# Optimization experiments

Hardware: AMD Instinct MI355X
Metric: run time of the kernel (lower is better)

The kernel has to match this reference:

```python
import jax, jax.numpy as jnp
import numpy as np

WIN = 8
NUM_LAYERS = 2
HID = 512
GROUPS = 4
GH = 2 * HID // GROUPS  # 256


def _shuffle(y):
    # torch Shuffle: transpose(-1,-2).contiguous().view(original_shape)
    return jnp.swapaxes(y, -1, -2).reshape(y.shape)


def _gru_cell(xt, h, w_ih, w_hh, b_ih, b_hh):
    # torch.nn.GRUCell math; gate order r, z, n
    gi = xt @ w_ih.T + b_ih  # [B, 3H]
    gh = h @ w_hh.T + b_hh   # [B, 3H]
    i_r, i_z, i_n = jnp.split(gi, 3, axis=1)
    h_r, h_z, h_n = jnp.split(gh, 3, axis=1)
    r = jax.nn.sigmoid(i_r + h_r)
    z = jax.nn.sigmoid(i_z + h_z)
    n = jnp.tanh(i_n + r * h_n)
    return (1.0 - z) * n + z * h


def _sort_attn(h, a1, a2, a3, a4):
    B, H = h.shape
    s = jnp.sort(h, axis=1)                 # stable sort along features
    se = jnp.stack((h, s), axis=1)          # [B, 2, H]
    y = se @ a1.T                           # Linear(H, H) -> [B, 2, H]
    y = y.reshape(B, GROUPS, GH)            # Flatten + Unflatten
    y = _shuffle(y)
    y = y @ a2.T                            # Linear(GH, GH)
    y = _shuffle(y)
    y = jax.nn.relu(y @ a3.T)               # Linear(GH, GH) + ReLU
    y = y.reshape(B, GROUPS * GH)           # [B, 2H]
    scores = jax.nn.sigmoid(y @ a4.T)       # Linear(2H, H) -> [B, H]
    return h * scores


def setup_inputs() -> dict:
    key = jax.random.key(0)
    ks = jax.random.split(key, 10)
    B, L, C = 64, 4096, 64
    sc = 0.05
    inp = {
        "x": jax.random.normal(ks[0], (B, L, C), dtype=jnp.float32),
        "hidden0": jnp.zeros((NUM_LAYERS, 1, HID), dtype=jnp.float32),
        "w_ih": jax.random.normal(ks[1], (NUM_LAYERS, 3 * HID, HID), dtype=jnp.float32) * sc,
        "w_hh": jax.random.normal(ks[2], (NUM_LAYERS, 3 * HID, HID), dtype=jnp.float32) * sc,
        "b_ih": jax.random.normal(ks[3], (NUM_LAYERS, 3 * HID), dtype=jnp.float32) * sc,
        "b_hh": jax.random.normal(ks[4], (NUM_LAYERS, 3 * HID), dtype=jnp.float32) * sc,
        "a1": jax.random.normal(ks[5], (NUM_LAYERS, HID, HID), dtype=jnp.float32) * sc,
        "a2": jax.random.normal(ks[6], (NUM_LAYERS, GH, GH), dtype=jnp.float32) * sc,
        "a3": jax.random.normal(ks[7], (NUM_LAYERS, GH, GH), dtype=jnp.float32) * sc,
        "a4": jax.random.normal(ks[8], (NUM_LAYERS, HID, 2 * HID), dtype=jnp.float32) * sc,
    }
    return inp


def reference(x, hidden0, w_ih, w_hh, b_ih, b_hh, a1, a2, a3, a4):
    B, L, C = x.shape
    xp = x.reshape(B, L // WIN, WIN * C)
    xs = jnp.swapaxes(xp, 0, 1)                       # [T, B, D]
    h0 = jnp.broadcast_to(hidden0, (NUM_LAYERS, B, HID))

    def step(hid, xt):
        inp = xt
        new = []
        for l in range(NUM_LAYERS):
            h = _gru_cell(inp, hid[l], w_ih[l], w_hh[l], b_ih[l], b_hh[l])
            h = _sort_attn(h, a1[l], a2[l], a3[l], a4[l])
            new.append(h)
            inp = h
        return jnp.stack(new, axis=0), inp

    _, outs = jax.lax.scan(step, h0, xs)              # outs: [T, B, H]
    return jnp.swapaxes(outs, 0, 1)                   # [B, T, H]
```

## Files before the change

### kernel.cpp

```cpp
#include <hip/hip_runtime.h>

#define SCOPE_AGENT __HIP_MEMORY_SCOPE_AGENT

#define OFF_HS    0
#define OFF_HP    65536
#define OFF_SG    131072
#define OFF_U     196608
#define OFF_CTR   327680
#define OFF_T1    393216
#define OFF_M     2490368
#define OFF_GIX   4587520
#define OFF_XT    4587520
#define WS_GIX    54919168
#define WS_XT     21364736

__device__ __forceinline__ float sigm(float x) { return 1.f / (1.f + expf(-x)); }

__device__ __forceinline__ float ld_sc1(const float* p) {
    return __hip_atomic_load(p, __ATOMIC_RELAXED, SCOPE_AGENT);
}
__device__ __forceinline__ void st_sc1(float* p, float v) {
    __hip_atomic_store(p, v, __ATOMIC_RELAXED, SCOPE_AGENT);
}
__device__ __forceinline__ void ld2(const float* p, float& a, float& b) {
    unsigned long long v = __hip_atomic_load((const unsigned long long*)p,
                                             __ATOMIC_RELAXED, SCOPE_AGENT);
    a = __uint_as_float((unsigned)v);
    b = __uint_as_float((unsigned)(v >> 32));
}
__device__ __forceinline__ void st2(float* p, float a, float b) {
    unsigned long long v = ((unsigned long long)__float_as_uint(b) << 32) |
                           (unsigned long long)__float_as_uint(a);
    __hip_atomic_store((unsigned long long*)p, v, __ATOMIC_RELAXED, SCOPE_AGENT);
}

__device__ __forceinline__ void gbar(unsigned* flags, unsigned* genr, unsigned g) {
    __syncthreads();
    const int tid = threadIdx.x;
    if (blockIdx.x == 0) {
        if (tid >= 1 && tid < 256) {
            while (__hip_atomic_load(&flags[tid << 5], __ATOMIC_RELAXED, SCOPE_AGENT) < g)
                __builtin_amdgcn_s_sleep(1);
        }
        __syncthreads();
        if (tid < 16)
            __hip_atomic_store(&genr[tid << 5], g, __ATOMIC_RELAXED, SCOPE_AGENT);
        __syncthreads();
    } else {
        if (tid == 0) {
            __hip_atomic_store(&flags[blockIdx.x << 5], g, __ATOMIC_RELAXED, SCOPE_AGENT);
            while (__hip_atomic_load(&genr[(blockIdx.x & 15) << 5], __ATOMIC_RELAXED, SCOPE_AGENT) < g)
                __builtin_amdgcn_s_sleep(1);
        }
        __syncthreads();
    }
}

__global__ void k_init(const float* __restrict__ h0, float* __restrict__ ws) {
    int idx = blockIdx.x * blockDim.x + threadIdx.x;
    int l = idx >> 15, k = (idx & 32767) >> 6, lane = idx & 63;
    ws[OFF_HS + (l << 15) + ((k >> 1) << 7) + (lane << 1) + (k & 1)] = h0[(l << 9) + k];
    if (idx < 8704) ((unsigned*)(ws + OFF_CTR))[idx] = 0u;
}

__global__ void k_gix(const float* __restrict__ x, const float* __restrict__ wih,
                      float* __restrict__ gix) {
    __shared__ float xs[128][65];
    __shared__ float ww[32][129];
    int t = blockIdx.x, rb = blockIdx.y * 32;
    int tid = threadIdx.x;
    int rw = tid >> 6, b = tid & 63;
    float acc[8] = {0.f, 0.f, 0.f, 0.f, 0.f, 0.f, 0.f, 0.f};
    for (int kc = 0; kc < 4; kc++) {
        __syncthreads();
        for (int i = tid; i < 8192; i += 256) {
            int k = i & 127, b2 = i >> 7;
            xs[k][b2] = x[(size_t)b2 * 262144 + (size_t)t * 512 + kc * 128 + k];
        }
        for (int i = tid; i < 4096; i += 256) {
            int r = i >> 7, k = i & 127;
            ww[r][k] = wih[(size_t)(rb + r) * 512 + kc * 128 + k];
        }
        __syncthreads();
        for (int k = 0; k < 128; k++) {
            float xv = xs[k][b];
#pragma unroll
            for (int rr = 0; rr < 8; rr++)
                acc[rr] = fmaf(ww[rw * 8 + rr][k], xv, acc[rr]);
        }
    }
#pragma unroll
    for (int rr = 0; rr < 8; rr++) {
        int rg = rb + rw * 8 + rr;
        int g = rg >> 9, j = rg & 511;
        gix[((size_t)((size_t)t * 512 + j) * 3 + g) * 64 + b] = acc[rr];
    }
}

__global__ void k_xtk(const float* __restrict__ x, float* __restrict__ xT) {
    __shared__ float tile[64][65];
    int t = blockIdx.x >> 3, kc = blockIdx.x & 7;
    int k = threadIdx.x & 63, b0 = threadIdx.x >> 6;
    for (int i = 0; i < 16; i++) {
        int b = i * 4 + b0;
        tile[k][b] = x[(size_t)b * 262144 + (size_t)t * 512 + kc * 64 + k];
    }
    __syncthreads();
    int b2 = threadIdx.x & 63, k0 = threadIdx.x >> 6;
    for (int i = 0; i < 16; i++) {
        int k2 = i * 4 + k0;
        xT[((size_t)t * 512 + kc * 64 + k2) * 64 + b2] = tile[k2][b2];
    }
}

__global__ void k_t1(const float* __restrict__ a1, const float* __restrict__ a2,
                     float* __restrict__ T1) {
    int l = blockIdx.x >> 10, c = blockIdx.x & 1023;
    int g = c >> 8, jj = c & 255;
    __shared__ float sA2[256];
    sA2[threadIdx.x] = a2[l * 65536 + jj * 256 + threadIdx.x];
    __syncthreads();
    const float* A1l = a1 + l * 262144;
    for (int colq = 0; colq < 4; colq++) {
        int col = colq * 256 + threadIdx.x;
        int half = col >> 9, cm = col & 511;
        float acc = 0.f;
#pragma unroll 4
        for (int q = 0; q < 64; q++) {
            int a0 = 2 * half;
            int j0 = g * 64 + q;
            acc = fmaf(sA2[4 * q + a0],     A1l[j0 * 512 + cm], acc);
            acc = fmaf(sA2[4 * q + a0 + 1], A1l[(j0 + 256) * 512 + cm], acc);
        }
        T1[((size_t)(l << 10) + c) * 1024 + col] = acc;
    }
}

__global__ void k_m(const float* __restrict__ a3, const float* __restrict__ T1,
                    float* __restrict__ M) {
    int l = blockIdx.x >> 10, c = blockIdx.x & 1023;
    int g = c >> 8, jj = c & 255;
    __shared__ float sA3[256];
    sA3[threadIdx.x] = a3[l * 65536 + jj * 256 + threadIdx.x];
    __syncthreads();
    const float* T1l = T1 + ((size_t)l << 20);
    for (int colq = 0; colq < 4; colq++) {
        int col = colq * 256 + threadIdx.x;
        float acc = 0.f;
#pragma unroll 4
        for (int m = 0; m < 256; m++) {
            int p = ((m & 3) << 8) + (g << 6) + (m >> 2);
            acc = fmaf(sA3[m], T1l[p * 1024 + col], acc);
        }
        M[((size_t)(l << 10) + c) * 1024 + col] = acc;
    }
}

__global__ void __launch_bounds__(1024, 1)
persist(const float* __restrict__ x, const float* __restrict__ xT,
        const float* __restrict__ gix, int has_xt, int has_gix,
        const float* __restrict__ wih, const float* __restrict__ whh,
        const float* __restrict__ bih, const float* __restrict__ bhh,
        const float* __restrict__ Mc, const float* __restrict__ a4,
        float* __restrict__ ws, float* __restrict__ out) {
    __shared__ float wA[2][2][6][512];
    __shared__ float wM[2][4][1024];
    __shared__ float wD[2][2][1024];
    __shared__ float red2[12][16][64];
    __shared__ float bb[2][2][4];
    __shared__ float sH[2][2][64];

    const int tid = threadIdx.x, w = tid >> 6, lane = tid & 63, bid = blockIdx.x;

    for (int i = tid; i < 12288; i += 1024) {
        int l = i / 6144, r = i % 6144, f = r / 3072, r2 = r % 3072, d = r2 / 512, k = r2 & 511;
        int gate = d >> 1, side = d & 1;
        int j = 2 * bid + f;
        const float* src = side ? whh : wih;
        wA[l][f][d][k] = src[l * 786432 + (gate * 512 + j) * 512 + k];
    }
    for (int i = tid; i < 8192; i += 1024) {
        int l = i >> 12, r = (i >> 10) & 3, col = i & 1023;
        wM[l][r][col] = Mc[((size_t)(l << 10) + 4 * bid + r) * 1024 + col];
    }
    for (int i = tid; i < 4096; i += 1024) {
        int l = i >> 11, f = (i >> 10) & 1, k = i & 1023;
        wD[l][f][k] = a4[l * 524288 + (2 * bid + f) * 1024 + k];
    }
    if (tid < 16) {
        int l = tid / 8, f = (tid / 4) & 1, g = tid & 3;
        int j = 2 * bid + f;
        float v;
        if (g == 0)      v = bih[l * 1536 + j] + bhh[l * 1536 + j];
        else if (g == 1) v = bih[l * 1536 + 512 + j] + bhh[l * 1536 + 512 + j];
        else if (g == 2) v = bih[l * 1536 + 1024 + j];
        else             v = bhh[l * 1536 + 1024 + j];
        bb[l][f][g] = v;
    }
    __syncthreads();

    float* hsG = ws + OFF_HS;
    float* hPg = ws + OFF_HP;
    float* sGg = ws + OFF_SG;
    float* uG  = ws + OFF_U;
    unsigned* flags = (unsigned*)(ws + OFF_CTR);
    unsigned* genr  = flags + 8192;
    unsigned bgen = 0;

    auto stageA = [&](int l, int t) {
        float hprev = 0.f;
        if (w < 2) {
            int j = 2 * bid + w;
            hprev = ld_sc1(&hsG[(l << 15) + ((j >> 1) << 7) + (lane << 1) + (j & 1)]);
        }
        const float* hb = hsG + (l << 15);
        float* hPl = hPg + (l << 15);
        int k0 = w * 32;
        if (l == 0 && has_gix) {
            float acc[6] = {0.f, 0.f, 0.f, 0.f, 0.f, 0.f};
#pragma unroll 8
            for (int m = 0; m < 16; m++) {
                int k = k0 + 2 * m;
                float ha, hb2;
                ld2(&hb[(k >> 1) * 128 + lane * 2], ha, hb2);
#pragma unroll
                for (int f = 0; f < 2; f++) {
                    acc[f * 3 + 0] = fmaf(wA[0][f][1][k], ha, fmaf(wA[0][f][1][k + 1], hb2, acc[f * 3 + 0]));
                    acc[f * 3 + 1] = fmaf(wA[0][f][3][k], ha, fmaf(wA[0][f][3][k + 1], hb2, acc[f * 3 + 1]));
                    acc[f * 3 + 2] = fmaf(wA[0][f][5][k], ha, fmaf(wA[0][f][5][k + 1], hb2, acc[f * 3 + 2]));
                }
            }
#pragma unroll
            for (int u = 0; u < 6; u++) red2[u][w][lane] = acc[u];
            __syncthreads();
            if (w < 2) {
                int f = w, j = 2 * bid + f;
                float s0 = 0, s1 = 0, s2 = 0;
#pragma unroll
                for (int i = 0; i < 16; i++) {
                    s0 += red2[f * 3 + 0][i][lane];
                    s1 += red2[f * 3 + 1][i][lane];
                    s2 += red2[f * 3 + 2][i][lane];
                }
                const float* gx = gix + ((size_t)((size_t)t * 512 + j) * 3) * 64;
                float r = sigm(gx[lane] + s0 + bb[0][f][0]);
                float z = sigm(gx[64 + lane] + s1 + bb[0][f][1]);
                float n = tanhf(gx[128 + lane] + bb[0][f][2] + r * (s2 + bb[0][f][3]));
                float hp = (1.f - z) * n + z * hprev;
                sH[0][f][lane] = hp;
                st_sc1(&hPl[bid * 128 + lane * 2 + f], hp);
            }
        } else {
            float acc[12];
#pragma unroll
            for (int u = 0; u < 12; u++) acc[u] = 0.f;
#pragma unroll 8
            for (int m = 0; m < 16; m++) {
                int k = k0 + 2 * m;
                float ia, ib, ha, hb2;
                if (l == 1) {
                    ld2(&hsG[(k >> 1) * 128 + lane * 2], ia, ib);
                } else if (has_xt) {
                    ia = xT[(size_t)t * 32768 + k * 64 + lane];
                    ib = xT[(size_t)t * 32768 + (k + 1) * 64 + lane];
                } else {
                    ia = x[(size_t)lane * 262144 + (size_t)t * 512 + k];
                    ib = x[(size_t)lane * 262144 + (size_t)t * 512 + k + 1];
                }
                ld2(&hb[(k >> 1) * 128 + lane * 2], ha, hb2);
#pragma unroll
                for (int f = 0; f < 2; f++) {
                    acc[f * 6 + 0] = fmaf(wA[l][f][0][k], ia, fmaf(wA[l][f][0][k + 1], ib, acc[f * 6 + 0]));
                    acc[f * 6 + 1] = fmaf(wA[l][f][1][k], ha, fmaf(wA[l][f][1][k + 1], hb2, acc[f * 6 + 1]));
                    acc[f * 6 + 2] = fmaf(wA[l][f][2][k], ia, fmaf(wA[l][f][2][k + 1], ib, acc[f * 6 + 2]));
                    acc[f * 6 + 3] = fmaf(wA[l][f][3][k], ha, fmaf(wA[l][f][3][k + 1], hb2, acc[f * 6 + 3]));
                    acc[f * 6 + 4] = fmaf(wA[l][f][4][k], ia, fmaf(wA[l][f][4][k + 1], ib, acc[f * 6 + 4]));
                    acc[f * 6 + 5] = fmaf(wA[l][f][5][k], ha, fmaf(wA[l][f][5][k + 1], hb2, acc[f * 6 + 5]));
                }
            }
#pragma unroll
            for (int u = 0; u < 12; u++) red2[u][w][lane] = acc[u];
            __syncthreads();
            if (w < 2) {
                int f = w, j = 2 * bid + f;
                float g0 = 0, g1 = 0, g2 = 0, g3 = 0, g4 = 0, g5 = 0;
#pragma unroll
                for (int i = 0; i < 16; i++) {
                    g0 += red2[f * 6 + 0][i][lane]; g1 += red2[f * 6 + 1][i][lane];
                    g2 += red2[f * 6 + 2][i][lane]; g3 += red2[f * 6 + 3][i][lane];
                    g4 += red2[f * 6 + 4][i][lane]; g5 += red2[f * 6 + 5][i][lane];
                }
                float r = sigm(g0 + g1 + bb[l][f][0]);
                float z = sigm(g2 + g3 + bb[l][f][1]);
                float n = tanhf(g4 + bb[l][f][2] + r * (g5 + bb[l][f][3]));
                float hp = (1.f - z) * n + z * hprev;
                sH[l][f][lane] = hp;
                st_sc1(&hPl[bid * 128 + lane * 2 + f], hp);
            }
        }
    };

    auto stageB = [&](int l, float* accB) {
        int j0 = 2 * bid, j1 = j0 + 1;
        float v0 = sH[l][0][lane], v1 = sH[l][1][lane];
        const float* hPl = hPg + (l << 15);
        float* sGl = sGg + (l << 15);
        int k0 = w * 32, cnt0 = 0, cnt1 = 0;
        accB[0] = accB[1] = accB[2] = accB[3] = 0.f;
#pragma unroll 8
        for (int m = 0; m < 16; m++) {
            int k = k0 + 2 * m;
            float ha, hb2;
            ld2(&hPl[(k >> 1) * 128 + lane * 2], ha, hb2);
            cnt0 += (ha < v0 || (ha == v0 && k < j0)) ? 1 : 0;
            cnt0 += (hb2 < v0 || (hb2 == v0 && k + 1 < j0)) ? 1 : 0;
            cnt1 += (ha < v1 || (ha == v1 && k < j1)) ? 1 : 0;
            cnt1 += (hb2 < v1 || (hb2 == v1 && k + 1 < j1)) ? 1 : 0;
#pragma unroll
            for (int r = 0; r < 4; r++)
                accB[r] = fmaf(wM[l][r][k], ha, fmaf(wM[l][r][k + 1], hb2, accB[r]));
        }
        red2[0][w][lane] = (float)cnt0;
        red2[1][w][lane] = (float)cnt1;
        __syncthreads();
        if (w < 2) {
            int rk = 0;
#pragma unroll
            for (int i = 0; i < 16; i++) rk += (int)red2[w][i][lane];
            st_sc1(&sGl[rk * 64 + lane], sH[l][w][lane]);
        }
    };

    auto stageC = [&](int l, const float* accB) {
        float acc[4] = {accB[0], accB[1], accB[2], accB[3]};
        int s0 = w * 32;
        const float* sGl = sGg + (l << 15);
#pragma unroll 8
        for (int ss = 0; ss < 32; ss++) {
            int sp = s0 + ss;
            float vv = ld_sc1(&sGl[sp * 64 + lane]);
#pragma unroll
            for (int r = 0; r < 4; r++)
                acc[r] = fmaf(wM[l][r][512 + sp], vv, acc[r]);
        }
#pragma unroll
        for (int r = 0; r < 4; r++) red2[r][w][lane] = acc[r];
        __syncthreads();
        if (w < 2) {
            float sa = 0.f, sb = 0.f;
#pragma unroll
            for (int i = 0; i < 16; i++) {
                sa += red2[2 * w + 0][i][lane];
                sb += red2[2 * w + 1][i][lane];
            }
            st2(&uG[(l << 16) + (2 * bid + w) * 128 + lane * 2],
                fmaxf(sa, 0.f), fmaxf(sb, 0.f));
        }
    };

    auto stageD = [&](int l, int t) {
        float a0 = 0.f, a1v = 0.f;
        int k0 = w * 64;
        const float* uL = uG + (l << 16);
#pragma unroll 8
        for (int m = 0; m < 32; m++) {
            int k = k0 + 2 * m;
            float ua, ub;
            ld2(&uL[(k >> 1) * 128 + lane * 2], ua, ub);
            a0 = fmaf(wD[l][0][k], ua, fmaf(wD[l][0][k + 1], ub, a0));
            a1v = fmaf(wD[l][1][k], ua, fmaf(wD[l][1][k + 1], ub, a1v));
        }
        red2[0][w][lane] = a0;
        red2[1][w][lane] = a1v;
        __syncthreads();
        if (w < 2) {
            float s = 0.f;
#pragma unroll
            for (int i = 0; i < 16; i++) s += red2[w][i][lane];
            float hnew = sH[l][w][lane] * sigm(s);
            int j = 2 * bid + w;
            st_sc1(&hsG[(l << 15) + bid * 128 + lane * 2 + w], hnew);
            if (l == 1)
                out[(size_t)lane * 262144 + (size_t)t * 512 + j] = hnew;
        }
    };

    float accB0[4], accB1[4];

    for (int t = 0; t <= 512; t++) {
        const int t0 = t, t1 = t - 1;
        const bool do0 = (t0 < 512), do1 = (t1 >= 0);

        if (do0) stageA(0, t0);
        if (do1) { __syncthreads(); stageA(1, t1); }
        gbar(flags, genr, ++bgen);

        if (do0) stageB(0, accB0);
        if (do1) { __syncthreads(); stageB(1, accB1); }
        gbar(flags, genr, ++bgen);

        if (do0) stageC(0, accB0);
        if (do1) { __syncthreads(); stageC(1, accB1); }
        gbar(flags, genr, ++bgen);

        if (do0) stageD(0, t0);
        if (do1) { __syncthreads(); stageD(1, t1); }
        gbar(flags, genr, ++bgen);
    }
}

extern "C" void kernel_launch(void* const* d_in, const int* in_sizes, int n_in,
                              void* d_out, int out_size, void* d_ws, size_t ws_size,
                              hipStream_t stream) {
    const float* x   = (const float*)d_in[0];
    const float* h0  = (const float*)d_in[1];
    const float* wih = (const float*)d_in[2];
    const float* whh = (const float*)d_in[3];
    const float* bih = (const float*)d_in[4];
    const float* bhh = (const float*)d_in[5];
    const float* a1  = (const float*)d_in[6];
    const float* a2  = (const float*)d_in[7];
    const float* a3  = (const float*)d_in[8];
    const float* a4  = (const float*)d_in[9];
    float* ws  = (float*)d_ws;
    float* out = (float*)d_out;

    int has_gix = (ws_size >= (size_t)WS_GIX * 4) ? 1 : 0;
    int has_xt  = (!has_gix && ws_size >= (size_t)WS_XT * 4) ? 1 : 0;
    float* T1p = ws + OFF_T1;
    float* Mp  = ws + OFF_M;
    const float* gixp = ws + OFF_GIX;
    const float* xTp  = ws + OFF_XT;

    hipLaunchKernelGGL(k_init, dim3(256), dim3(256), 0, stream, h0, ws);
    if (has_gix)
        hipLaunchKernelGGL(k_gix, dim3(512, 48), dim3(256), 0, stream, x, wih, ws + OFF_GIX);
    else if (has_xt)
        hipLaunchKernelGGL(k_xtk, dim3(4096), dim3(256), 0, stream, x, ws + OFF_XT);
    hipLaunchKernelGGL(k_t1, dim3(2048), dim3(256), 0, stream, a1, a2, T1p);
    hipLaunchKernelGGL(k_m, dim3(2048), dim3(256), 0, stream, a3, T1p, Mp);

    void* args[] = {(void*)&x, (void*)&xTp, (void*)&gixp, (void*)&has_xt, (void*)&has_gix,
                    (void*)&wih, (void*)&whh, (void*)&bih, (void*)&bhh,
                    (void*)&Mp, (void*)&a4, (void*)&ws, (void*)&out};
    hipLaunchCooperativeKernel((void*)persist, dim3(256), dim3(1024), args, 0, stream);
}
```

Measured before the change: 45.07 ms.

## Switch global state buffers to 4-wide interleaved layout with batched dwordx4 loads

Changes the layout of the hidden-state, sorted and intermediate global buffers from pairs of features per lane to groups of four. Each stage now issues eight coherent global_load_dwordx4 loads at once through inline asm with a single wait, instead of a serialized loop of 64-bit atomic loads. The aim is to cut memory-latency round trips in the latency-bound persistent recurrent loop. It adds register pressure from holding 32 floats per load batch, and the launch-bounds hint is changed from 1 to 4.

```diff
diff --git a/kernel.cpp b/kernel.cpp
--- a/kernel.cpp
+++ b/kernel.cpp
@@ -14,6 +14,8 @@
 #define WS_GIX    54919168
 #define WS_XT     21364736
 
+typedef float f32x4 __attribute__((ext_vector_type(4)));
+
 __device__ __forceinline__ float sigm(float x) { return 1.f / (1.f + expf(-x)); }
 
 __device__ __forceinline__ float ld_sc1(const float* p) {
@@ -21,17 +23,29 @@
 }
 __device__ __forceinline__ void st_sc1(float* p, float v) {
     __hip_atomic_store(p, v, __ATOMIC_RELAXED, SCOPE_AGENT);
-}
-__device__ __forceinline__ void ld2(const float* p, float& a, float& b) {
-    unsigned long long v = __hip_atomic_load((const unsigned long long*)p,
-                                             __ATOMIC_RELAXED, SCOPE_AGENT);
-    a = __uint_as_float((unsigned)v);
-    b = __uint_as_float((unsigned)(v >> 32));
 }
 __device__ __forceinline__ void st2(float* p, float a, float b) {
     unsigned long long v = ((unsigned long long)__float_as_uint(b) << 32) |
                            (unsigned long long)__float_as_uint(a);
     __hip_atomic_store((unsigned long long*)p, v, __ATOMIC_RELAXED, SCOPE_AGENT);
+}
+
+__device__ __forceinline__ void ld4b8(const float* base, f32x4* v) {
+    const float* b2 = base + 1024;
+    asm volatile(
+        "global_load_dwordx4 %0, %8, off sc0 sc1\n\t"
+        "global_load_dwordx4 %1, %8, off offset:1024 sc0 sc1\n\t"
+        "global_load_dwordx4 %2, %8, off offset:2048 sc0 sc1\n\t"
+        "global_load_dwordx4 %3, %8, off offset:3072 sc0 sc1\n\t"
+        "global_load_dwordx4 %4, %9, off sc0 sc1\n\t"
+        "global_load_dwordx4 %5, %9, off offset:1024 sc0 sc1\n\t"
+        "global_load_dwordx4 %6, %9, off offset:2048 sc0 sc1\n\t"
+        "global_load_dwordx4 %7, %9, off offset:3072 sc0 sc1\n\t"
+        "s_waitcnt vmcnt(0)"
+        : "=&v"(v[0]), "=&v"(v[1]), "=&v"(v[2]), "=&v"(v[3]),
+          "=&v"(v[4]), "=&v"(v[5]), "=&v"(v[6]), "=&v"(v[7])
+        : "v"(base), "v"(b2)
+        : "memory");
 }
 
 __device__ __forceinline__ void gbar(unsigned* flags, unsigned* genr, unsigned g) {
@@ -59,7 +73,7 @@
 __global__ void k_init(const float* __restrict__ h0, float* __restrict__ ws) {
     int idx = blockIdx.x * blockDim.x + threadIdx.x;
     int l = idx >> 15, k = (idx & 32767) >> 6, lane = idx & 63;
-    ws[OFF_HS + (l << 15) + ((k >> 1) << 7) + (lane << 1) + (k & 1)] = h0[(l << 9) + k];
+    ws[OFF_HS + (l << 15) + ((k >> 2) << 8) + (lane << 2) + (k & 3)] = h0[(l << 9) + k];
     if (idx < 8704) ((unsigned*)(ws + OFF_CTR))[idx] = 0u;
 }
 
@@ -108,8 +122,8 @@
     __syncthreads();
     int b2 = threadIdx.x & 63, k0 = threadIdx.x >> 6;
     for (int i = 0; i < 16; i++) {
-        int k2 = i * 4 + k0;
-        xT[((size_t)t * 512 + kc * 64 + k2) * 64 + b2] = tile[k2][b2];
+        int k2 = kc * 64 + i * 4 + k0;
+        xT[(size_t)t * 32768 + ((k2 >> 2) << 8) + (b2 << 2) + (k2 & 3)] = tile[i * 4 + k0][b2];
     }
 }
 
@@ -156,7 +170,7 @@
     }
 }
 
-__global__ void __launch_bounds__(1024, 1)
+__global__ void __launch_bounds__(1024, 4)
 persist(const float* __restrict__ x, const float* __restrict__ xT,
         const float* __restrict__ gix, int has_xt, int has_gix,
         const float* __restrict__ wih, const float* __restrict__ whh,
@@ -211,23 +225,27 @@
         float hprev = 0.f;
         if (w < 2) {
             int j = 2 * bid + w;
-            hprev = ld_sc1(&hsG[(l << 15) + ((j >> 1) << 7) + (lane << 1) + (j & 1)]);
+            hprev = ld_sc1(&hsG[(l << 15) + ((j >> 2) << 8) + (lane << 2) + (j & 3)]);
         }
         const float* hb = hsG + (l << 15);
         float* hPl = hPg + (l << 15);
         int k0 = w * 32;
         if (l == 0 && has_gix) {
             float acc[6] = {0.f, 0.f, 0.f, 0.f, 0.f, 0.f};
-#pragma unroll 8
-            for (int m = 0; m < 16; m++) {
-                int k = k0 + 2 * m;
-                float ha, hb2;
-                ld2(&hb[(k >> 1) * 128 + lane * 2], ha, hb2);
-#pragma unroll
-                for (int f = 0; f < 2; f++) {
-                    acc[f * 3 + 0] = fmaf(wA[0][f][1][k], ha, fmaf(wA[0][f][1][k + 1], hb2, acc[f * 3 + 0]));
-                    acc[f * 3 + 1] = fmaf(wA[0][f][3][k], ha, fmaf(wA[0][f][3][k + 1], hb2, acc[f * 3 + 1]));
-                    acc[f * 3 + 2] = fmaf(wA[0][f][5][k], ha, fmaf(wA[0][f][5][k + 1], hb2, acc[f * 3 + 2]));
+            f32x4 hv[8];
+            ld4b8(hb + ((k0 >> 2) << 8) + (lane << 2), hv);
+#pragma unroll
+            for (int m = 0; m < 8; m++) {
+#pragma unroll
+                for (int q = 0; q < 4; q++) {
+                    int k = k0 + 4 * m + q;
+                    float h = hv[m][q];
+#pragma unroll
+                    for (int f = 0; f < 2; f++) {
+                        acc[f * 3 + 0] = fmaf(wA[0][f][1][k], h, acc[f * 3 + 0]);
+                        acc[f * 3 + 1] = fmaf(wA[0][f][3][k], h, acc[f * 3 + 1]);
+                        acc[f * 3 + 2] = fmaf(wA[0][f][5][k], h, acc[f * 3 + 2]);
+                    }
                 }
             }
 #pragma unroll
@@ -248,34 +266,56 @@
                 float n = tanhf(gx[128 + lane] + bb[0][f][2] + r * (s2 + bb[0][f][3]));
                 float hp = (1.f - z) * n + z * hprev;
                 sH[0][f][lane] = hp;
-                st_sc1(&hPl[bid * 128 + lane * 2 + f], hp);
+                st_sc1(&hPl[((j >> 2) << 8) + (lane << 2) + (j & 3)], hp);
             }
         } else {
             float acc[12];
 #pragma unroll
             for (int u = 0; u < 12; u++) acc[u] = 0.f;
-#pragma unroll 8
-            for (int m = 0; m < 16; m++) {
-                int k = k0 + 2 * m;
-                float ia, ib, ha, hb2;
+            {
+                f32x4 iv[8];
                 if (l == 1) {
-                    ld2(&hsG[(k >> 1) * 128 + lane * 2], ia, ib);
+                    ld4b8(hsG + ((k0 >> 2) << 8) + (lane << 2), iv);
                 } else if (has_xt) {
-                    ia = xT[(size_t)t * 32768 + k * 64 + lane];
-                    ib = xT[(size_t)t * 32768 + (k + 1) * 64 + lane];
+                    ld4b8(xT + (size_t)t * 32768 + ((k0 >> 2) << 8) + (lane << 2), iv);
                 } else {
-                    ia = x[(size_t)lane * 262144 + (size_t)t * 512 + k];
-                    ib = x[(size_t)lane * 262144 + (size_t)t * 512 + k + 1];
-                }
-                ld2(&hb[(k >> 1) * 128 + lane * 2], ha, hb2);
-#pragma unroll
-                for (int f = 0; f < 2; f++) {
-                    acc[f * 6 + 0] = fmaf(wA[l][f][0][k], ia, fmaf(wA[l][f][0][k + 1], ib, acc[f * 6 + 0]));
-                    acc[f * 6 + 1] = fmaf(wA[l][f][1][k], ha, fmaf(wA[l][f][1][k + 1], hb2, acc[f * 6 + 1]));
-                    acc[f * 6 + 2] = fmaf(wA[l][f][2][k], ia, fmaf(wA[l][f][2][k + 1], ib, acc[f * 6 + 2]));
-                    acc[f * 6 + 3] = fmaf(wA[l][f][3][k], ha, fmaf(wA[l][f][3][k + 1], hb2, acc[f * 6 + 3]));
-                    acc[f * 6 + 4] = fmaf(wA[l][f][4][k], ia, fmaf(wA[l][f][4][k + 1], ib, acc[f * 6 + 4]));
-                    acc[f * 6 + 5] = fmaf(wA[l][f][5][k], ha, fmaf(wA[l][f][5][k + 1], hb2, acc[f * 6 + 5]));
+#pragma unroll
+                    for (int m = 0; m < 8; m++)
+#pragma unroll
+                        for (int q = 0; q < 4; q++)
+                            iv[m][q] = x[(size_t)lane * 262144 + (size_t)t * 512 + k0 + 4 * m + q];
+                }
+#pragma unroll
+                for (int m = 0; m < 8; m++) {
+#pragma unroll
+                    for (int q = 0; q < 4; q++) {
+                        int k = k0 + 4 * m + q;
+                        float ivq = iv[m][q];
+#pragma unroll
+                        for (int f = 0; f < 2; f++) {
+                            acc[f * 6 + 0] = fmaf(wA[l][f][0][k], ivq, acc[f * 6 + 0]);
+                            acc[f * 6 + 2] = fmaf(wA[l][f][2][k], ivq, acc[f * 6 + 2]);
+                            acc[f * 6 + 4] = fmaf(wA[l][f][4][k], ivq, acc[f * 6 + 4]);
+                        }
+                    }
+                }
+            }
+            {
+                f32x4 hv[8];
+                ld4b8(hb + ((k0 >> 2) << 8) + (lane << 2), hv);
+#pragma unroll
+                for (int m = 0; m < 8; m++) {
+#pragma unroll
+                    for (int q = 0; q < 4; q++) {
+                        int k = k0 + 4 * m + q;
+                        float h = hv[m][q];
+#pragma unroll
+                        for (int f = 0; f < 2; f++) {
+                            acc[f * 6 + 1] = fmaf(wA[l][f][1][k], h, acc[f * 6 + 1]);
+                            acc[f * 6 + 3] = fmaf(wA[l][f][3][k], h, acc[f * 6 + 3]);
+                            acc[f * 6 + 5] = fmaf(wA[l][f][5][k], h, acc[f * 6 + 5]);
+                        }
+                    }
                 }
             }
 #pragma unroll
@@ -295,7 +335,7 @@
                 float n = tanhf(g4 + bb[l][f][2] + r * (g5 + bb[l][f][3]));
                 float hp = (1.f - z) * n + z * hprev;
                 sH[l][f][lane] = hp;
-                st_sc1(&hPl[bid * 128 + lane * 2 + f], hp);
+                st_sc1(&hPl[((j >> 2) << 8) + (lane << 2) + (j & 3)], hp);
             }
         }
     };
@@ -307,18 +347,20 @@
         float* sGl = sGg + (l << 15);
         int k0 = w * 32, cnt0 = 0, cnt1 = 0;
         accB[0] = accB[1] = accB[2] = accB[3] = 0.f;
-#pragma unroll 8
-        for (int m = 0; m < 16; m++) {
-            int k = k0 + 2 * m;
-            float ha, hb2;
-            ld2(&hPl[(k >> 1) * 128 + lane * 2], ha, hb2);
-            cnt0 += (ha < v0 || (ha == v0 && k < j0)) ? 1 : 0;
-            cnt0 += (hb2 < v0 || (hb2 == v0 && k + 1 < j0)) ? 1 : 0;
-            cnt1 += (ha < v1 || (ha == v1 && k < j1)) ? 1 : 0;
-            cnt1 += (hb2 < v1 || (hb2 == v1 && k + 1 < j1)) ? 1 : 0;
-#pragma unroll
-            for (int r = 0; r < 4; r++)
-                accB[r] = fmaf(wM[l][r][k], ha, fmaf(wM[l][r][k + 1], hb2, accB[r]));
+        f32x4 hv[8];
+        ld4b8(hPl + ((k0 >> 2) << 8) + (lane << 2), hv);
+#pragma unroll
+        for (int m = 0; m < 8; m++) {
+#pragma unroll
+            for (int q = 0; q < 4; q++) {
+                int k = k0 + 4 * m + q;
+                float h = hv[m][q];
+                cnt0 += (h < v0 || (h == v0 && k < j0)) ? 1 : 0;
+                cnt1 += (h < v1 || (h == v1 && k < j1)) ? 1 : 0;
+#pragma unroll
+                for (int r = 0; r < 4; r++)
+                    accB[r] = fmaf(wM[l][r][k], h, accB[r]);
+            }
         }
         red2[0][w][lane] = (float)cnt0;
         red2[1][w][lane] = (float)cnt1;
@@ -327,7 +369,7 @@
             int rk = 0;
 #pragma unroll
             for (int i = 0; i < 16; i++) rk += (int)red2[w][i][lane];
-            st_sc1(&sGl[rk * 64 + lane], sH[l][w][lane]);
+            st_sc1(&sGl[((rk >> 2) << 8) + (lane << 2) + (rk & 3)], sH[l][w][lane]);
         }
     };
 
@@ -335,13 +377,18 @@
         float acc[4] = {accB[0], accB[1], accB[2], accB[3]};
         int s0 = w * 32;
         const float* sGl = sGg + (l << 15);
-#pragma unroll 8
-        for (int ss = 0; ss < 32; ss++) {
-            int sp = s0 + ss;
-            float vv = ld_sc1(&sGl[sp * 64 + lane]);
-#pragma unroll
-            for (int r = 0; r < 4; r++)
-                acc[r] = fmaf(wM[l][r][512 + sp], vv, acc[r]);
+        f32x4 sv[8];
+        ld4b8(sGl + ((s0 >> 2) << 8) + (lane << 2), sv);
+#pragma unroll
+        for (int m = 0; m < 8; m++) {
+#pragma unroll
+            for (int q = 0; q < 4; q++) {
+                int sp = s0 + 4 * m + q;
+                float vv = sv[m][q];
+#pragma unroll
+                for (int r = 0; r < 4; r++)
+                    acc[r] = fmaf(wM[l][r][512 + sp], vv, acc[r]);
+            }
         }
 #pragma unroll
         for (int r = 0; r < 4; r++) red2[r][w][lane] = acc[r];
@@ -353,7 +400,7 @@
                 sa += red2[2 * w + 0][i][lane];
                 sb += red2[2 * w + 1][i][lane];
             }
-            st2(&uG[(l << 16) + (2 * bid + w) * 128 + lane * 2],
+            st2(&uG[(l << 16) + (bid << 8) + (lane << 2) + (w << 1)],
                 fmaxf(sa, 0.f), fmaxf(sb, 0.f));
         }
     };
@@ -362,13 +409,29 @@
         float a0 = 0.f, a1v = 0.f;
         int k0 = w * 64;
         const float* uL = uG + (l << 16);
-#pragma unroll 8
-        for (int m = 0; m < 32; m++) {
-            int k = k0 + 2 * m;
-            float ua, ub;
-            ld2(&uL[(k >> 1) * 128 + lane * 2], ua, ub);
-            a0 = fmaf(wD[l][0][k], ua, fmaf(wD[l][0][k + 1], ub, a0));
-            a1v = fmaf(wD[l][1][k], ua, fmaf(wD[l][1][k + 1], ub, a1v));
+        {
+            f32x4 uv[8];
+            ld4b8(uL + ((k0 >> 2) << 8) + (lane << 2), uv);
+#pragma unroll
+            for (int m = 0; m < 8; m++)
+#pragma unroll
+                for (int q = 0; q < 4; q++) {
+                    int k = k0 + 4 * m + q;
+                    a0 = fmaf(wD[l][0][k], uv[m][q], a0);
+                    a1v = fmaf(wD[l][1][k], uv[m][q], a1v);
+                }
+        }
+        {
+            f32x4 uv[8];
+            ld4b8(uL + (((k0 >> 2) + 8) << 8) + (lane << 2), uv);
+#pragma unroll
+            for (int m = 0; m < 8; m++)
+#pragma unroll
+                for (int q = 0; q < 4; q++) {
+                    int k = k0 + 32 + 4 * m + q;
+                    a0 = fmaf(wD[l][0][k], uv[m][q], a0);
+                    a1v = fmaf(wD[l][1][k], uv[m][q], a1v);
+                }
         }
         red2[0][w][lane] = a0;
         red2[1][w][lane] = a1v;
@@ -379,7 +442,7 @@
             for (int i = 0; i < 16; i++) s += red2[w][i][lane];
             float hnew = sH[l][w][lane] * sigm(s);
             int j = 2 * bid + w;
-            st_sc1(&hsG[(l << 15) + bid * 128 + lane * 2 + w], hnew);
+            st_sc1(&hsG[(l << 15) + ((j >> 2) << 8) + (lane << 2) + (j & 3)], hnew);
             if (l == 1)
                 out[(size_t)lane * 262144 + (size_t)t * 512 + j] = hnew;
         }
```

After: 48.50 ms. 1.08x slower.
